# Performance work log

Measured on AMD Instinct MI355X. Metric: run time of the kernel, lower is better.

## Reference

```python
import jax, jax.numpy as jnp
import numpy as np

B, C, H, W = 1, 8192, 32, 32
C8 = C // 8  # 1024 == H*W; required by the (b,hw,hw)/(b,c8) broadcast in the original code


def setup_inputs() -> dict:
    key = jax.random.key(0)
    ks = jax.random.split(key, 11)
    rn = lambda i, shape, s=1.0: jax.random.normal(ks[i], shape, dtype=jnp.float32) * s
    return {
        "x": rn(0, (B, C, H, W)),
        "Wq": rn(1, (C8, C), 0.02),
        "Wk": rn(2, (C8, C), 0.02),
        "Wv": rn(3, (C, C), 0.02),
        "q_scale": jax.random.uniform(ks[4], (C8,), minval=0.5, maxval=1.5),
        "q_shift": rn(5, (C8,), 0.1),
        "k_scale": jax.random.uniform(ks[6], (C8,), minval=0.5, maxval=1.5),
        "k_shift": rn(7, (C8,), 0.1),
        "v_scale": jax.random.uniform(ks[8], (C,), minval=0.5, maxval=1.5),
        "v_shift": rn(9, (C,), 0.1),
        "gamma": rn(10, (), 0.5),
    }


def reference(x, Wq, Wk, Wv, q_scale, q_shift, k_scale, k_shift, v_scale, v_shift, gamma):
    b, c, h, w = x.shape
    n = h * w
    xf = x.reshape(b, c, n)  # (b, c, n)
    # BasicConv2d = 1x1 conv (no bias) + BatchNorm2d; BN folded to per-channel scale/shift
    q = jnp.einsum('oc,bcn->bon', Wq, xf) * q_scale[:, None] + q_shift[:, None]  # (b, c8, n)
    k = jnp.einsum('oc,bcn->bon', Wk, xf) * k_scale[:, None] + k_shift[:, None]  # (b, c8, n)
    v = jnp.einsum('oc,bcn->bon', Wv, xf) * v_scale[:, None] + v_shift[:, None]  # (b, c,  n)
    q = q.transpose(0, 2, 1)  # (b, n, c8)
    # PPMCC score: per-channel centering, covariance across channels
    q_c = q - q.mean(axis=1, keepdims=True)
    k_c = k - k.mean(axis=2, keepdims=True)
    cov = jnp.einsum('bnc,bcm->bnm', q_c, k_c) / (n - 1)  # (b, n, n)
    q_std = q.std(axis=1)  # (b, c8), ddof=0 (matches torch unbiased=False)
    k_std = k.std(axis=2)  # (b, c8)
    ppmcc = cov / (q_std * k_std)  # broadcasts over last axis since c8 == n
    att = jax.nn.softmax(ppmcc, axis=-1).transpose(0, 2, 1)  # (b, n, n)
    out = jnp.einsum('bcn,bnm->bcm', v, att).reshape(b, c, h, w)
    return gamma * out + x
```

## Files before the change

kernel.cpp:

```cpp
#include <hip/hip_runtime.h>
#include <cstdint>
#include <cstddef>

#define CDIM 8192
#define NDIM 1024
#define C8D  1024

typedef __bf16 bf16_t;
typedef __bf16 bf16x8 __attribute__((ext_vector_type(8)));
typedef __bf16 bf16x4 __attribute__((ext_vector_type(4)));
typedef float  f32x4  __attribute__((ext_vector_type(4)));

__device__ __forceinline__ void gload_lds16(const void* g, void* l) {
    __builtin_amdgcn_global_load_lds((const __attribute__((address_space(1))) void*)g,
                                     (__attribute__((address_space(3))) void*)l, 16, 0, 0);
}

__global__ __launch_bounds__(256) void cvt_bf16_k(const float* __restrict__ in,
                                                  bf16_t* __restrict__ out, int n8) {
    int idx = blockIdx.x * 256 + threadIdx.x;
    int stride = gridDim.x * 256;
    for (int i = idx; i < n8; i += stride) {
        size_t off = (size_t)i * 8;
        float4 a = *(const float4*)(in + off);
        float4 b = *(const float4*)(in + off + 4);
        bf16x8 o = { (__bf16)a.x, (__bf16)a.y, (__bf16)a.z, (__bf16)a.w,
                     (__bf16)b.x, (__bf16)b.y, (__bf16)b.z, (__bf16)b.w };
        *(bf16x8*)(out + off) = o;
    }
}

__global__ __launch_bounds__(256) void transpose_cvt_x(const float* __restrict__ x,
                                                       bf16_t* __restrict__ xT) {
    __shared__ float t[32][33];
    const int n0 = blockIdx.x * 32, c0 = blockIdx.y * 32;
    const int tx = threadIdx.x, ty = threadIdx.y;
    #pragma unroll
    for (int i = 0; i < 4; ++i)
        t[ty + i * 8][tx] = x[(size_t)(c0 + ty + i * 8) * NDIM + n0 + tx];
    __syncthreads();
    #pragma unroll
    for (int i = 0; i < 4; ++i)
        xT[(size_t)(n0 + ty + i * 8) * CDIM + c0 + tx] = (__bf16)t[tx][ty + i * 8];
}

__global__ __launch_bounds__(256) void mega_gemm(
    const bf16_t* __restrict__ Wv, const bf16_t* __restrict__ Wq,
    const bf16_t* __restrict__ Wk, const bf16_t* __restrict__ Bx,
    bf16_t* __restrict__ v_out, float* __restrict__ q_out, float* __restrict__ k_out,
    const float* __restrict__ v_scale, const float* __restrict__ v_shift,
    const float* __restrict__ q_scale, const float* __restrict__ q_shift,
    const float* __restrict__ k_scale, const float* __restrict__ k_shift)
{
    const int gx = gridDim.x;
    const int nwg = gx * gridDim.y;
    const int lin = blockIdx.y * gx + blockIdx.x;
    const int tile = (lin & 7) * (nwg >> 3) + (lin >> 3);
    const int row0 = (tile / gx) * 128;
    const int col0 = (tile % gx) * 128;

    const bf16_t* A; const float* s0; const float* s1;
    int arow; int path;
    if (row0 < 8192)      { A = Wv; arow = row0;        s0 = v_scale; s1 = v_shift; path = 0; }
    else if (row0 < 9216) { A = Wq; arow = row0 - 8192; s0 = q_scale; s1 = q_shift; path = 1; }
    else                  { A = Wk; arow = row0 - 9216; s0 = k_scale; s1 = k_shift; path = 2; }

    const int tid = threadIdx.x;
    __shared__ __align__(16) bf16_t As[128 * 32];
    __shared__ __align__(16) bf16_t Bs[128 * 32];

    const int lane = tid & 63;
    const int w    = tid >> 6;
    const int wm   = (w >> 1) * 64;
    const int wn   = (w & 1) * 64;
    const int lr   = lane & 15;
    const int kg   = (lane >> 4) * 8;

    f32x4 acc[4][4];
    #pragma unroll
    for (int a_ = 0; a_ < 4; ++a_)
        #pragma unroll
        for (int b_ = 0; b_ < 4; ++b_)
            acc[a_][b_] = (f32x4){0.f, 0.f, 0.f, 0.f};

    const int eA = tid * 8;
    const int eB = (256 + tid) * 8;
    const int rA = eA >> 5, cA = eA & 31;
    const int rB = eB >> 5, cB = eB & 31;

    for (int kb = 0; kb < CDIM; kb += 32) {
        gload_lds16(A + (size_t)(arow + rA) * CDIM + kb + cA, As + eA);
        gload_lds16(A + (size_t)(arow + rB) * CDIM + kb + cB, As + eB);
        gload_lds16(Bx + (size_t)(col0 + rA) * CDIM + kb + cA, Bs + eA);
        gload_lds16(Bx + (size_t)(col0 + rB) * CDIM + kb + cB, Bs + eB);
        __syncthreads();

        bf16x8 av[4], bv[4];
        #pragma unroll
        for (int mi = 0; mi < 4; ++mi)
            av[mi] = *(const bf16x8*)(As + (wm + mi * 16 + lr) * 32 + kg);
        #pragma unroll
        for (int ni = 0; ni < 4; ++ni)
            bv[ni] = *(const bf16x8*)(Bs + (wn + ni * 16 + lr) * 32 + kg);

        #pragma unroll
        for (int mi = 0; mi < 4; ++mi)
            #pragma unroll
            for (int ni = 0; ni < 4; ++ni)
                acc[mi][ni] = __builtin_amdgcn_mfma_f32_16x16x32_bf16(
                    av[mi], bv[ni], acc[mi][ni], 0, 0, 0);
        __syncthreads();
    }

    const int cr = (lane >> 4) * 4;
    #pragma unroll
    for (int mi = 0; mi < 4; ++mi) {
        #pragma unroll
        for (int ni = 0; ni < 4; ++ni) {
            const int j = col0 + wn + ni * 16 + lr;
            #pragma unroll
            for (int r = 0; r < 4; ++r) {
                const int il = arow + wm + mi * 16 + cr + r;
                float v = acc[mi][ni][r] * s0[il] + s1[il];
                if (path == 0)      v_out[(size_t)il * NDIM + j] = (__bf16)v;
                else if (path == 1) q_out[(size_t)il * NDIM + j] = v;
                else                k_out[(size_t)il * NDIM + j] = v;
            }
        }
    }
}

template <int EPI, typename OutT>
__global__ __launch_bounds__(256) void gemm_bt(
    const bf16_t* __restrict__ A, const bf16_t* __restrict__ B,
    OutT* __restrict__ C, int M, int N, int K,
    const float* __restrict__ e0, const float* __restrict__ e1,
    const float* __restrict__ gs)
{
    const int gx = gridDim.x;
    const int nwg = gx * gridDim.y;
    const int lin = blockIdx.y * gx + blockIdx.x;
    int tile = lin;
    if ((nwg & 7) == 0) tile = (lin & 7) * (nwg >> 3) + (lin >> 3);
    const int row0 = (tile / gx) * 128;
    const int col0 = (tile % gx) * 128;

    const int tid = threadIdx.x;
    __shared__ __align__(16) bf16_t As[128 * 32];
    __shared__ __align__(16) bf16_t Bs[128 * 32];

    const int lane = tid & 63;
    const int w    = tid >> 6;
    const int wm   = (w >> 1) * 64;
    const int wn   = (w & 1) * 64;
    const int lr   = lane & 15;
    const int kg   = (lane >> 4) * 8;

    f32x4 acc[4][4];
    #pragma unroll
    for (int a_ = 0; a_ < 4; ++a_)
        #pragma unroll
        for (int b_ = 0; b_ < 4; ++b_)
            acc[a_][b_] = (f32x4){0.f, 0.f, 0.f, 0.f};

    const int eA = tid * 8;
    const int eB = (256 + tid) * 8;
    const int rA = eA >> 5, cA = eA & 31;
    const int rB = eB >> 5, cB = eB & 31;

    for (int kb = 0; kb < K; kb += 32) {
        gload_lds16(A + (size_t)(row0 + rA) * K + kb + cA, As + eA);
        gload_lds16(A + (size_t)(row0 + rB) * K + kb + cB, As + eB);
        gload_lds16(B + (size_t)(col0 + rA) * K + kb + cA, Bs + eA);
        gload_lds16(B + (size_t)(col0 + rB) * K + kb + cB, Bs + eB);
        __syncthreads();

        bf16x8 av[4], bv[4];
        #pragma unroll
        for (int mi = 0; mi < 4; ++mi)
            av[mi] = *(const bf16x8*)(As + (wm + mi * 16 + lr) * 32 + kg);
        #pragma unroll
        for (int ni = 0; ni < 4; ++ni)
            bv[ni] = *(const bf16x8*)(Bs + (wn + ni * 16 + lr) * 32 + kg);

        #pragma unroll
        for (int mi = 0; mi < 4; ++mi)
            #pragma unroll
            for (int ni = 0; ni < 4; ++ni)
                acc[mi][ni] = __builtin_amdgcn_mfma_f32_16x16x32_bf16(
                    av[mi], bv[ni], acc[mi][ni], 0, 0, 0);
        __syncthreads();
    }

    float g = 0.f;
    if (EPI == 3) g = gs[0];
    const int cr = (lane >> 4) * 4;
    #pragma unroll
    for (int mi = 0; mi < 4; ++mi) {
        #pragma unroll
        for (int ni = 0; ni < 4; ++ni) {
            const int j = col0 + wn + ni * 16 + lr;
            float s0 = 0.f, s1 = 0.f;
            if (EPI == 2) { s0 = e0[j]; s1 = e1[j]; }
            #pragma unroll
            for (int r = 0; r < 4; ++r) {
                const int i = row0 + wm + mi * 16 + cr + r;
                float v = acc[mi][ni][r];
                if (EPI == 2)      v = v * (1.0f / 1023.0f) / (s0 * s1);
                else if (EPI == 3) v = g * v + e0[(size_t)i * N + j];
                C[(size_t)i * N + j] = (OutT)v;
            }
        }
    }
}

__global__ __launch_bounds__(256) void rowstats(
    const float* __restrict__ Q, const float* __restrict__ Km,
    float* __restrict__ qmean, float* __restrict__ qstd,
    float* __restrict__ kmean, float* __restrict__ kstd)
{
    const int wid  = blockIdx.x * 4 + (threadIdx.x >> 6);
    const int lane = threadIdx.x & 63;
    const float* src = (wid < 1024) ? (Q + (size_t)wid * NDIM)
                                    : (Km + (size_t)(wid - 1024) * NDIM);
    float s = 0.f, s2 = 0.f;
    #pragma unroll
    for (int p = 0; p < 4; ++p) {
        float4 v = *(const float4*)(src + p * 256 + lane * 4);
        s  += v.x + v.y + v.z + v.w;
        s2 += v.x * v.x + v.y * v.y + v.z * v.z + v.w * v.w;
    }
    #pragma unroll
    for (int o = 32; o; o >>= 1) { s += __shfl_xor(s, o); s2 += __shfl_xor(s2, o); }
    if (lane == 0) {
        float m   = s / 1024.f;
        float var = fmaxf(s2 / 1024.f - m * m, 0.f);
        if (wid < 1024) { qmean[wid] = m; qstd[wid] = sqrtf(var); }
        else            { kmean[wid - 1024] = m; kstd[wid - 1024] = sqrtf(var); }
    }
}

__global__ __launch_bounds__(256) void center_tr(
    const float* __restrict__ Q, const float* __restrict__ qmu, bf16_t* __restrict__ qc,
    const float* __restrict__ Km, const float* __restrict__ kmu, bf16_t* __restrict__ kc)
{
    __shared__ float t[32][33];
    const float* M  = blockIdx.z ? Km  : Q;
    const float* mu = blockIdx.z ? kmu : qmu;
    bf16_t* O       = blockIdx.z ? kc  : qc;
    const int o0 = blockIdx.y * 32, n0 = blockIdx.x * 32;
    const int tx = threadIdx.x, ty = threadIdx.y;
    #pragma unroll
    for (int i = 0; i < 4; ++i) {
        const int o = o0 + ty + i * 8;
        t[ty + i * 8][tx] = M[(size_t)o * NDIM + n0 + tx] - mu[o];
    }
    __syncthreads();
    #pragma unroll
    for (int i = 0; i < 4; ++i)
        O[(size_t)(n0 + ty + i * 8) * C8D + o0 + tx] = (__bf16)t[tx][ty + i * 8];
}

__global__ __launch_bounds__(256) void softmax_rows(const float* __restrict__ P,
                                                    bf16_t* __restrict__ O) {
    const int row = blockIdx.x;
    const int tid = threadIdx.x;
    const float4 v = ((const float4*)(P + (size_t)row * NDIM))[tid];
    float mx = fmaxf(fmaxf(v.x, v.y), fmaxf(v.z, v.w));
    #pragma unroll
    for (int o = 32; o; o >>= 1) mx = fmaxf(mx, __shfl_xor(mx, o));
    __shared__ float red[8];
    const int w = tid >> 6, lane = tid & 63;
    if (lane == 0) red[w] = mx;
    __syncthreads();
    mx = fmaxf(fmaxf(red[0], red[1]), fmaxf(red[2], red[3]));
    float e0 = __expf(v.x - mx), e1 = __expf(v.y - mx);
    float e2 = __expf(v.z - mx), e3 = __expf(v.w - mx);
    float s = e0 + e1 + e2 + e3;
    #pragma unroll
    for (int o = 32; o; o >>= 1) s += __shfl_xor(s, o);
    if (lane == 0) red[4 + w] = s;
    __syncthreads();
    s = red[4] + red[5] + red[6] + red[7];
    const float inv = 1.0f / s;
    bf16x4 o4 = { (__bf16)(e0 * inv), (__bf16)(e1 * inv),
                  (__bf16)(e2 * inv), (__bf16)(e3 * inv) };
    ((bf16x4*)(O + (size_t)row * NDIM))[tid] = o4;
}

extern "C" void kernel_launch(void* const* d_in, const int* in_sizes, int n_in,
                              void* d_out, int out_size, void* d_ws, size_t ws_size,
                              hipStream_t stream)
{
    const float* x       = (const float*)d_in[0];
    const float* Wq      = (const float*)d_in[1];
    const float* Wk      = (const float*)d_in[2];
    const float* Wv      = (const float*)d_in[3];
    const float* q_scale = (const float*)d_in[4];
    const float* q_shift = (const float*)d_in[5];
    const float* k_scale = (const float*)d_in[6];
    const float* k_shift = (const float*)d_in[7];
    const float* v_scale = (const float*)d_in[8];
    const float* v_shift = (const float*)d_in[9];
    const float* gamma   = (const float*)d_in[10];
    float* out = (float*)d_out;

    char* w = (char*)d_ws;
    bf16_t* Wv_b = (bf16_t*)w; w += (size_t)CDIM * CDIM * 2;
    bf16_t* Wq_b = (bf16_t*)w; w += (size_t)C8D  * CDIM * 2;
    bf16_t* Wk_b = (bf16_t*)w; w += (size_t)C8D  * CDIM * 2;
    bf16_t* xT   = (bf16_t*)w; w += (size_t)NDIM * CDIM * 2;
    bf16_t* v_b  = (bf16_t*)w; w += (size_t)CDIM * NDIM * 2;
    float*  q_on = (float*) w; w += (size_t)C8D * NDIM * 4;
    float*  k_on = (float*) w; w += (size_t)C8D * NDIM * 4;
    float*  P    = (float*) w; w += (size_t)NDIM * NDIM * 4;
    bf16_t* qc   = (bf16_t*)w; w += (size_t)NDIM * C8D * 2;
    bf16_t* kc   = (bf16_t*)w; w += (size_t)NDIM * C8D * 2;
    bf16_t* A0   = (bf16_t*)w; w += (size_t)NDIM * NDIM * 2;
    float*  qmean = (float*)w; w += C8D * 4;
    float*  qstd  = (float*)w; w += C8D * 4;
    float*  kmean = (float*)w; w += C8D * 4;
    float*  kstd  = (float*)w; w += C8D * 4;

    cvt_bf16_k<<<2048, 256, 0, stream>>>(Wv, Wv_b, (int)((size_t)CDIM * CDIM / 8));
    cvt_bf16_k<<<2048, 256, 0, stream>>>(Wq, Wq_b, C8D * CDIM / 8);
    cvt_bf16_k<<<2048, 256, 0, stream>>>(Wk, Wk_b, C8D * CDIM / 8);
    transpose_cvt_x<<<dim3(NDIM / 32, CDIM / 32), dim3(32, 8), 0, stream>>>(x, xT);

    mega_gemm<<<dim3(NDIM / 128, 10240 / 128), 256, 0, stream>>>(
        Wv_b, Wq_b, Wk_b, xT, v_b, q_on, k_on,
        v_scale, v_shift, q_scale, q_shift, k_scale, k_shift);

    rowstats<<<512, 256, 0, stream>>>(q_on, k_on, qmean, qstd, kmean, kstd);

    center_tr<<<dim3(32, 32, 2), dim3(32, 8), 0, stream>>>(
        q_on, qmean, qc, k_on, kmean, kc);

    gemm_bt<2, float><<<dim3(NDIM / 128, NDIM / 128), 256, 0, stream>>>(
        qc, kc, P, NDIM, NDIM, C8D, qstd, kstd, nullptr);

    softmax_rows<<<NDIM, 256, 0, stream>>>(P, A0);

    gemm_bt<3, float><<<dim3(NDIM / 128, CDIM / 128), 256, 0, stream>>>(
        v_b, A0, out, CDIM, NDIM, NDIM, x, x, gamma);
}
```

Baseline: 414.9 us.

## Add split-K to projection GEMM and score GEMM with separate reductions

The projection GEMM (10240x1024, K=8192) is split into two K halves over blockIdx.z, writing fp32 partials that a new reduce kernel sums and applies the BN scale/shift and bf16/fp32 conversion. The score GEMM (1024x1024, 64 tiles) is split 4-way in K, and its partials are summed inside softmax_rows. This raises workgroup counts to fill more CUs on small-tile-count GEMMs. The cost is extra fp32 partial traffic (about 80 MB for the projection) and an added kernel launch.

```diff
diff --git a/kernel.cpp b/kernel.cpp
--- a/kernel.cpp
+++ b/kernel.cpp
@@ -5,6 +5,7 @@
 #define CDIM 8192
 #define NDIM 1024
 #define C8D  1024
+#define MSTACK 10240
 
 typedef __bf16 bf16_t;
 typedef __bf16 bf16x8 __attribute__((ext_vector_type(8)));
@@ -47,23 +48,18 @@
 __global__ __launch_bounds__(256) void mega_gemm(
     const bf16_t* __restrict__ Wv, const bf16_t* __restrict__ Wq,
     const bf16_t* __restrict__ Wk, const bf16_t* __restrict__ Bx,
-    bf16_t* __restrict__ v_out, float* __restrict__ q_out, float* __restrict__ k_out,
-    const float* __restrict__ v_scale, const float* __restrict__ v_shift,
-    const float* __restrict__ q_scale, const float* __restrict__ q_shift,
-    const float* __restrict__ k_scale, const float* __restrict__ k_shift)
-{
-    const int gx = gridDim.x;
-    const int nwg = gx * gridDim.y;
-    const int lin = blockIdx.y * gx + blockIdx.x;
-    const int tile = (lin & 7) * (nwg >> 3) + (lin >> 3);
-    const int row0 = (tile / gx) * 128;
-    const int col0 = (tile % gx) * 128;
-
-    const bf16_t* A; const float* s0; const float* s1;
-    int arow; int path;
-    if (row0 < 8192)      { A = Wv; arow = row0;        s0 = v_scale; s1 = v_shift; path = 0; }
-    else if (row0 < 9216) { A = Wq; arow = row0 - 8192; s0 = q_scale; s1 = q_shift; path = 1; }
-    else                  { A = Wk; arow = row0 - 9216; s0 = k_scale; s1 = k_shift; path = 2; }
+    float* __restrict__ pp)
+{
+    const int z = blockIdx.z;
+    const int lin = blockIdx.y * 8 + blockIdx.x;
+    const int tile = (lin & 7) * 80 + (lin >> 3);
+    const int row0 = (tile >> 3) * 128;
+    const int col0 = (tile & 7) * 128;
+
+    const bf16_t* A; int arow;
+    if (row0 < 8192)      { A = Wv; arow = row0; }
+    else if (row0 < 9216) { A = Wq; arow = row0 - 8192; }
+    else                  { A = Wk; arow = row0 - 9216; }
 
     const int tid = threadIdx.x;
     __shared__ __align__(16) bf16_t As[128 * 32];
@@ -88,7 +84,9 @@
     const int rA = eA >> 5, cA = eA & 31;
     const int rB = eB >> 5, cB = eB & 31;
 
-    for (int kb = 0; kb < CDIM; kb += 32) {
+    const int kb0 = z * (CDIM / 2);
+    const int kb1 = kb0 + (CDIM / 2);
+    for (int kb = kb0; kb < kb1; kb += 32) {
         gload_lds16(A + (size_t)(arow + rA) * CDIM + kb + cA, As + eA);
         gload_lds16(A + (size_t)(arow + rB) * CDIM + kb + cB, As + eB);
         gload_lds16(Bx + (size_t)(col0 + rA) * CDIM + kb + cA, Bs + eA);
@@ -112,6 +110,7 @@
         __syncthreads();
     }
 
+    float* pz = pp + (size_t)z * MSTACK * NDIM;
     const int cr = (lane >> 4) * 4;
     #pragma unroll
     for (int mi = 0; mi < 4; ++mi) {
@@ -120,12 +119,43 @@
             const int j = col0 + wn + ni * 16 + lr;
             #pragma unroll
             for (int r = 0; r < 4; ++r) {
-                const int il = arow + wm + mi * 16 + cr + r;
-                float v = acc[mi][ni][r] * s0[il] + s1[il];
-                if (path == 0)      v_out[(size_t)il * NDIM + j] = (__bf16)v;
-                else if (path == 1) q_out[(size_t)il * NDIM + j] = v;
-                else                k_out[(size_t)il * NDIM + j] = v;
+                const int gi = row0 + wm + mi * 16 + cr + r;
+                pz[(size_t)gi * NDIM + j] = acc[mi][ni][r];
             }
+        }
+    }
+}
+
+__global__ __launch_bounds__(256) void reduce_mega(
+    const float* __restrict__ pp, bf16_t* __restrict__ v_out,
+    float* __restrict__ q_out, float* __restrict__ k_out,
+    const float* __restrict__ vs, const float* __restrict__ vh,
+    const float* __restrict__ qs, const float* __restrict__ qh,
+    const float* __restrict__ ks_, const float* __restrict__ kh)
+{
+    const size_t NU = (size_t)MSTACK * NDIM / 4;
+    const size_t stride = (size_t)gridDim.x * 256;
+    for (size_t u = (size_t)blockIdx.x * 256 + threadIdx.x; u < NU; u += stride) {
+        float4 a = ((const float4*)pp)[u];
+        float4 b = ((const float4*)pp)[u + NU];
+        const int i  = (int)(u >> 8);
+        const int jj = ((int)u & 255) * 4;
+        float sx = a.x + b.x, sy = a.y + b.y, sz = a.z + b.z, sw = a.w + b.w;
+        if (i < 8192) {
+            const float sc = vs[i], sh = vh[i];
+            bf16x4 o = { (__bf16)(sx * sc + sh), (__bf16)(sy * sc + sh),
+                         (__bf16)(sz * sc + sh), (__bf16)(sw * sc + sh) };
+            *(bf16x4*)(v_out + (size_t)i * NDIM + jj) = o;
+        } else if (i < 9216) {
+            const int il = i - 8192;
+            const float sc = qs[il], sh = qh[il];
+            float4 o = { sx * sc + sh, sy * sc + sh, sz * sc + sh, sw * sc + sh };
+            *(float4*)(q_out + (size_t)il * NDIM + jj) = o;
+        } else {
+            const int il = i - 9216;
+            const float sc = ks_[il], sh = kh[il];
+            float4 o = { sx * sc + sh, sy * sc + sh, sz * sc + sh, sw * sc + sh };
+            *(float4*)(k_out + (size_t)il * NDIM + jj) = o;
         }
     }
 }
@@ -145,6 +175,10 @@
     const int row0 = (tile / gx) * 128;
     const int col0 = (tile % gx) * 128;
 
+    const int Ks  = K / gridDim.z;
+    const int kb0 = blockIdx.z * Ks;
+    OutT* Cz = C + (size_t)blockIdx.z * M * N;
+
     const int tid = threadIdx.x;
     __shared__ __align__(16) bf16_t As[128 * 32];
     __shared__ __align__(16) bf16_t Bs[128 * 32];
@@ -168,7 +202,7 @@
     const int rA = eA >> 5, cA = eA & 31;
     const int rB = eB >> 5, cB = eB & 31;
 
-    for (int kb = 0; kb < K; kb += 32) {
+    for (int kb = kb0; kb < kb0 + Ks; kb += 32) {
         gload_lds16(A + (size_t)(row0 + rA) * K + kb + cA, As + eA);
         gload_lds16(A + (size_t)(row0 + rB) * K + kb + cB, As + eB);
         gload_lds16(B + (size_t)(col0 + rA) * K + kb + cA, Bs + eA);
@@ -208,7 +242,7 @@
                 float v = acc[mi][ni][r];
                 if (EPI == 2)      v = v * (1.0f / 1023.0f) / (s0 * s1);
                 else if (EPI == 3) v = g * v + e0[(size_t)i * N + j];
-                C[(size_t)i * N + j] = (OutT)v;
+                Cz[(size_t)i * N + j] = (OutT)v;
             }
         }
     }
@@ -265,7 +299,12 @@
                                                     bf16_t* __restrict__ O) {
     const int row = blockIdx.x;
     const int tid = threadIdx.x;
-    const float4 v = ((const float4*)(P + (size_t)row * NDIM))[tid];
+    const size_t PL = (size_t)NDIM * NDIM / 4;
+    const size_t u  = (size_t)row * (NDIM / 4) + tid;
+    const float4* B = (const float4*)P;
+    float4 p0 = B[u], p1 = B[u + PL], p2 = B[u + 2 * PL], p3 = B[u + 3 * PL];
+    float4 v = { p0.x + p1.x + p2.x + p3.x, p0.y + p1.y + p2.y + p3.y,
+                 p0.z + p1.z + p2.z + p3.z, p0.w + p1.w + p2.w + p3.w };
     float mx = fmaxf(fmaxf(v.x, v.y), fmaxf(v.z, v.w));
     #pragma unroll
     for (int o = 32; o; o >>= 1) mx = fmaxf(mx, __shfl_xor(mx, o));
@@ -313,34 +352,38 @@
     bf16_t* v_b  = (bf16_t*)w; w += (size_t)CDIM * NDIM * 2;
     float*  q_on = (float*) w; w += (size_t)C8D * NDIM * 4;
     float*  k_on = (float*) w; w += (size_t)C8D * NDIM * 4;
-    float*  P    = (float*) w; w += (size_t)NDIM * NDIM * 4;
-    bf16_t* qc   = (bf16_t*)w; w += (size_t)NDIM * C8D * 2;
-    bf16_t* kc   = (bf16_t*)w; w += (size_t)NDIM * C8D * 2;
-    bf16_t* A0   = (bf16_t*)w; w += (size_t)NDIM * NDIM * 2;
     float*  qmean = (float*)w; w += C8D * 4;
     float*  qstd  = (float*)w; w += C8D * 4;
     float*  kmean = (float*)w; w += C8D * 4;
     float*  kstd  = (float*)w; w += C8D * 4;
+    char* U = w;
+    float*  pp = (float*)U;
+    float*  P  = (float*)U;
+    bf16_t* qc = (bf16_t*)(U + (size_t)4 * NDIM * NDIM * 4);
+    bf16_t* kc = qc + (size_t)NDIM * C8D;
+    bf16_t* A0 = kc + (size_t)NDIM * C8D;
 
     cvt_bf16_k<<<2048, 256, 0, stream>>>(Wv, Wv_b, (int)((size_t)CDIM * CDIM / 8));
     cvt_bf16_k<<<2048, 256, 0, stream>>>(Wq, Wq_b, C8D * CDIM / 8);
     cvt_bf16_k<<<2048, 256, 0, stream>>>(Wk, Wk_b, C8D * CDIM / 8);
     transpose_cvt_x<<<dim3(NDIM / 32, CDIM / 32), dim3(32, 8), 0, stream>>>(x, xT);
 
-    mega_gemm<<<dim3(NDIM / 128, 10240 / 128), 256, 0, stream>>>(
-        Wv_b, Wq_b, Wk_b, xT, v_b, q_on, k_on,
-        v_scale, v_shift, q_scale, q_shift, k_scale, k_shift);
+    mega_gemm<<<dim3(8, MSTACK / 128, 2), 256, 0, stream>>>(
+        Wv_b, Wq_b, Wk_b, xT, pp);
+
+    reduce_mega<<<2560, 256, 0, stream>>>(
+        pp, v_b, q_on, k_on, v_scale, v_shift, q_scale, q_shift, k_scale, k_shift);
 
     rowstats<<<512, 256, 0, stream>>>(q_on, k_on, qmean, qstd, kmean, kstd);
 
     center_tr<<<dim3(32, 32, 2), dim3(32, 8), 0, stream>>>(
         q_on, qmean, qc, k_on, kmean, kc);
 
-    gemm_bt<2, float><<<dim3(NDIM / 128, NDIM / 128), 256, 0, stream>>>(
+    gemm_bt<2, float><<<dim3(NDIM / 128, NDIM / 128, 4), 256, 0, stream>>>(
         qc, kc, P, NDIM, NDIM, C8D, qstd, kstd, nullptr);
 
     softmax_rows<<<NDIM, 256, 0, stream>>>(P, A0);
 
-    gemm_bt<3, float><<<dim3(NDIM / 128, CDIM / 128), 256, 0, stream>>>(
+    gemm_bt<3, float><<<dim3(NDIM / 128, CDIM / 128, 1), 256, 0, stream>>>(
         v_b, A0, out, CDIM, NDIM, NDIM, x, x, gamma);
 }
```

Measured after the change: 517.7 us. +24.8%, slower.

## Double-buffer LDS in GEMMs and split-K the covariance GEMM with reduction in softmax

Applied to the files above, without the earlier changes.

Adds two-stage LDS double buffering to both the stacked projection GEMM and the generic bt GEMM, so the global-to-LDS loads for the next K slice are issued before the current slice's MFMAs and one barrier per iteration is dropped. The small 1024x1024 covariance GEMM now uses a 4-way split-K over gridDim.z, writing four partial planes that softmax sums on load. The projection GEMM's tile swizzle is hard-coded to constants. Double buffering doubles LDS per block, which may reduce occupancy. The split-K adds extra P traffic, and applying the EPI=2 scaling to each partial before summing is algebraically equivalent.

```diff
diff --git a/kernel.cpp b/kernel.cpp
--- a/kernel.cpp
+++ b/kernel.cpp
@@ -5,6 +5,7 @@
 #define CDIM 8192
 #define NDIM 1024
 #define C8D  1024
+#define MSTACK 10240
 
 typedef __bf16 bf16_t;
 typedef __bf16 bf16x8 __attribute__((ext_vector_type(8)));
@@ -52,12 +53,10 @@
     const float* __restrict__ q_scale, const float* __restrict__ q_shift,
     const float* __restrict__ k_scale, const float* __restrict__ k_shift)
 {
-    const int gx = gridDim.x;
-    const int nwg = gx * gridDim.y;
-    const int lin = blockIdx.y * gx + blockIdx.x;
-    const int tile = (lin & 7) * (nwg >> 3) + (lin >> 3);
-    const int row0 = (tile / gx) * 128;
-    const int col0 = (tile % gx) * 128;
+    const int lin = blockIdx.y * 8 + blockIdx.x;
+    const int tile = (lin & 7) * 80 + (lin >> 3);
+    const int row0 = (tile >> 3) * 128;
+    const int col0 = (tile & 7) * 128;
 
     const bf16_t* A; const float* s0; const float* s1;
     int arow; int path;
@@ -66,8 +65,8 @@
     else                  { A = Wk; arow = row0 - 9216; s0 = k_scale; s1 = k_shift; path = 2; }
 
     const int tid = threadIdx.x;
-    __shared__ __align__(16) bf16_t As[128 * 32];
-    __shared__ __align__(16) bf16_t Bs[128 * 32];
+    __shared__ __align__(16) bf16_t As[2 * 4096];
+    __shared__ __align__(16) bf16_t Bs[2 * 4096];
 
     const int lane = tid & 63;
     const int w    = tid >> 6;
@@ -88,20 +87,29 @@
     const int rA = eA >> 5, cA = eA & 31;
     const int rB = eB >> 5, cB = eB & 31;
 
+#define MEGA_STAGE(buf, kb)                                                        \
+    do {                                                                           \
+        gload_lds16(A  + (size_t)(arow + rA) * CDIM + (kb) + cA, As + (buf)*4096 + eA); \
+        gload_lds16(A  + (size_t)(arow + rB) * CDIM + (kb) + cB, As + (buf)*4096 + eB); \
+        gload_lds16(Bx + (size_t)(col0 + rA) * CDIM + (kb) + cA, Bs + (buf)*4096 + eA); \
+        gload_lds16(Bx + (size_t)(col0 + rB) * CDIM + (kb) + cB, Bs + (buf)*4096 + eB); \
+    } while (0)
+
+    MEGA_STAGE(0, 0);
+    __syncthreads();
+    int cur = 0;
     for (int kb = 0; kb < CDIM; kb += 32) {
-        gload_lds16(A + (size_t)(arow + rA) * CDIM + kb + cA, As + eA);
-        gload_lds16(A + (size_t)(arow + rB) * CDIM + kb + cB, As + eB);
-        gload_lds16(Bx + (size_t)(col0 + rA) * CDIM + kb + cA, Bs + eA);
-        gload_lds16(Bx + (size_t)(col0 + rB) * CDIM + kb + cB, Bs + eB);
-        __syncthreads();
+        if (kb + 32 < CDIM) MEGA_STAGE(cur ^ 1, kb + 32);
+        const bf16_t* Ac = As + cur * 4096;
+        const bf16_t* Bc = Bs + cur * 4096;
 
         bf16x8 av[4], bv[4];
         #pragma unroll
         for (int mi = 0; mi < 4; ++mi)
-            av[mi] = *(const bf16x8*)(As + (wm + mi * 16 + lr) * 32 + kg);
+            av[mi] = *(const bf16x8*)(Ac + (wm + mi * 16 + lr) * 32 + kg);
         #pragma unroll
         for (int ni = 0; ni < 4; ++ni)
-            bv[ni] = *(const bf16x8*)(Bs + (wn + ni * 16 + lr) * 32 + kg);
+            bv[ni] = *(const bf16x8*)(Bc + (wn + ni * 16 + lr) * 32 + kg);
 
         #pragma unroll
         for (int mi = 0; mi < 4; ++mi)
@@ -110,7 +118,9 @@
                 acc[mi][ni] = __builtin_amdgcn_mfma_f32_16x16x32_bf16(
                     av[mi], bv[ni], acc[mi][ni], 0, 0, 0);
         __syncthreads();
-    }
+        cur ^= 1;
+    }
+#undef MEGA_STAGE
 
     const int cr = (lane >> 4) * 4;
     #pragma unroll
@@ -145,9 +155,14 @@
     const int row0 = (tile / gx) * 128;
     const int col0 = (tile % gx) * 128;
 
+    const int Ks  = K / gridDim.z;
+    const int kb0 = blockIdx.z * Ks;
+    const int kb1 = kb0 + Ks;
+    OutT* Cz = C + (size_t)blockIdx.z * M * N;
+
     const int tid = threadIdx.x;
-    __shared__ __align__(16) bf16_t As[128 * 32];
-    __shared__ __align__(16) bf16_t Bs[128 * 32];
+    __shared__ __align__(16) bf16_t As[2 * 4096];
+    __shared__ __align__(16) bf16_t Bs[2 * 4096];
 
     const int lane = tid & 63;
     const int w    = tid >> 6;
@@ -168,20 +183,29 @@
     const int rA = eA >> 5, cA = eA & 31;
     const int rB = eB >> 5, cB = eB & 31;
 
-    for (int kb = 0; kb < K; kb += 32) {
-        gload_lds16(A + (size_t)(row0 + rA) * K + kb + cA, As + eA);
-        gload_lds16(A + (size_t)(row0 + rB) * K + kb + cB, As + eB);
-        gload_lds16(B + (size_t)(col0 + rA) * K + kb + cA, Bs + eA);
-        gload_lds16(B + (size_t)(col0 + rB) * K + kb + cB, Bs + eB);
-        __syncthreads();
+#define BT_STAGE(buf, kb)                                                       \
+    do {                                                                        \
+        gload_lds16(A + (size_t)(row0 + rA) * K + (kb) + cA, As + (buf)*4096 + eA); \
+        gload_lds16(A + (size_t)(row0 + rB) * K + (kb) + cB, As + (buf)*4096 + eB); \
+        gload_lds16(B + (size_t)(col0 + rA) * K + (kb) + cA, Bs + (buf)*4096 + eA); \
+        gload_lds16(B + (size_t)(col0 + rB) * K + (kb) + cB, Bs + (buf)*4096 + eB); \
+    } while (0)
+
+    BT_STAGE(0, kb0);
+    __syncthreads();
+    int cur = 0;
+    for (int kb = kb0; kb < kb1; kb += 32) {
+        if (kb + 32 < kb1) BT_STAGE(cur ^ 1, kb + 32);
+        const bf16_t* Ac = As + cur * 4096;
+        const bf16_t* Bc = Bs + cur * 4096;
 
         bf16x8 av[4], bv[4];
         #pragma unroll
         for (int mi = 0; mi < 4; ++mi)
-            av[mi] = *(const bf16x8*)(As + (wm + mi * 16 + lr) * 32 + kg);
+            av[mi] = *(const bf16x8*)(Ac + (wm + mi * 16 + lr) * 32 + kg);
         #pragma unroll
         for (int ni = 0; ni < 4; ++ni)
-            bv[ni] = *(const bf16x8*)(Bs + (wn + ni * 16 + lr) * 32 + kg);
+            bv[ni] = *(const bf16x8*)(Bc + (wn + ni * 16 + lr) * 32 + kg);
 
         #pragma unroll
         for (int mi = 0; mi < 4; ++mi)
@@ -190,7 +214,9 @@
                 acc[mi][ni] = __builtin_amdgcn_mfma_f32_16x16x32_bf16(
                     av[mi], bv[ni], acc[mi][ni], 0, 0, 0);
         __syncthreads();
-    }
+        cur ^= 1;
+    }
+#undef BT_STAGE
 
     float g = 0.f;
     if (EPI == 3) g = gs[0];
@@ -208,7 +234,7 @@
                 float v = acc[mi][ni][r];
                 if (EPI == 2)      v = v * (1.0f / 1023.0f) / (s0 * s1);
                 else if (EPI == 3) v = g * v + e0[(size_t)i * N + j];
-                C[(size_t)i * N + j] = (OutT)v;
+                Cz[(size_t)i * N + j] = (OutT)v;
             }
         }
     }
@@ -265,7 +291,12 @@
                                                     bf16_t* __restrict__ O) {
     const int row = blockIdx.x;
     const int tid = threadIdx.x;
-    const float4 v = ((const float4*)(P + (size_t)row * NDIM))[tid];
+    const size_t PL = (size_t)NDIM * NDIM / 4;
+    const size_t u  = (size_t)row * (NDIM / 4) + tid;
+    const float4* B = (const float4*)P;
+    float4 p0 = B[u], p1 = B[u + PL], p2 = B[u + 2 * PL], p3 = B[u + 3 * PL];
+    float4 v = { p0.x + p1.x + p2.x + p3.x, p0.y + p1.y + p2.y + p3.y,
+                 p0.z + p1.z + p2.z + p3.z, p0.w + p1.w + p2.w + p3.w };
     float mx = fmaxf(fmaxf(v.x, v.y), fmaxf(v.z, v.w));
     #pragma unroll
     for (int o = 32; o; o >>= 1) mx = fmaxf(mx, __shfl_xor(mx, o));
@@ -313,7 +344,7 @@
     bf16_t* v_b  = (bf16_t*)w; w += (size_t)CDIM * NDIM * 2;
     float*  q_on = (float*) w; w += (size_t)C8D * NDIM * 4;
     float*  k_on = (float*) w; w += (size_t)C8D * NDIM * 4;
-    float*  P    = (float*) w; w += (size_t)NDIM * NDIM * 4;
+    float*  P    = (float*) w; w += (size_t)4 * NDIM * NDIM * 4;
     bf16_t* qc   = (bf16_t*)w; w += (size_t)NDIM * C8D * 2;
     bf16_t* kc   = (bf16_t*)w; w += (size_t)NDIM * C8D * 2;
     bf16_t* A0   = (bf16_t*)w; w += (size_t)NDIM * NDIM * 2;
@@ -327,7 +358,7 @@
     cvt_bf16_k<<<2048, 256, 0, stream>>>(Wk, Wk_b, C8D * CDIM / 8);
     transpose_cvt_x<<<dim3(NDIM / 32, CDIM / 32), dim3(32, 8), 0, stream>>>(x, xT);
 
-    mega_gemm<<<dim3(NDIM / 128, 10240 / 128), 256, 0, stream>>>(
+    mega_gemm<<<dim3(8, MSTACK / 128), 256, 0, stream>>>(
         Wv_b, Wq_b, Wk_b, xT, v_b, q_on, k_on,
         v_scale, v_shift, q_scale, q_shift, k_scale, k_shift);
 
@@ -336,11 +367,11 @@
     center_tr<<<dim3(32, 32, 2), dim3(32, 8), 0, stream>>>(
         q_on, qmean, qc, k_on, kmean, kc);
 
-    gemm_bt<2, float><<<dim3(NDIM / 128, NDIM / 128), 256, 0, stream>>>(
+    gemm_bt<2, float><<<dim3(NDIM / 128, NDIM / 128, 4), 256, 0, stream>>>(
         qc, kc, P, NDIM, NDIM, C8D, qstd, kstd, nullptr);
 
     softmax_rows<<<NDIM, 256, 0, stream>>>(P, A0);
 
-    gemm_bt<3, float><<<dim3(NDIM / 128, CDIM / 128), 256, 0, stream>>>(
+    gemm_bt<3, float><<<dim3(NDIM / 128, CDIM / 128, 1), 256, 0, stream>>>(
         v_b, A0, out, CDIM, NDIM, NDIM, x, x, gamma);
 }
```

New measurement: 418.8 us. No clear change (+0.9%).
